# Performance work log

Hardware: AMD Instinct MI355X
Metric: run time of the kernel (lower is better)

The kernel has to match this reference:

```python
import jax, jax.numpy as jnp
import numpy as np

B, S, D, H = 2, 1024, 768, 12
HD = D // H          # head_dim = 64
DFF = 4 * D          # 3072
EPS = 1e-5


def _ln(x, g, b):
    m = x.mean(-1, keepdims=True)
    v = ((x - m) ** 2).mean(-1, keepdims=True)
    return (x - m) * jax.lax.rsqrt(v + EPS) * g + b


def setup_inputs() -> dict:
    key = jax.random.key(0)
    ks = jax.random.split(key, 8)
    w = lambda k, shape: jax.random.normal(k, shape, jnp.float32) * 0.02
    return {
        "inp": jax.random.normal(ks[0], (B, S, D), jnp.float32),
        "attention_mask": jnp.zeros((B, S), bool),  # True = masked out (filled with -inf)
        "rel_matrix": jax.random.randint(ks[1], (B, S, S), -1, 2, jnp.int32),  # values in {-1,0,1}
        "qkv_w": w(ks[2], (3 * D, D)),
        "rel_A": w(ks[3], (3, HD)),        # relative_position_emb_A.weight
        "o_w": w(ks[4], (D, D)),
        "w1": w(ks[5], (DFF, D)), "b1": jnp.zeros((DFF,), jnp.float32),
        "w2": w(ks[6], (D, DFF)), "b2": jnp.zeros((D,), jnp.float32),
        "ln1_g": jnp.ones((D,), jnp.float32), "ln1_b": jnp.zeros((D,), jnp.float32),
        "ln2_g": jnp.ones((D,), jnp.float32), "ln2_b": jnp.zeros((D,), jnp.float32),
    }


def reference(inp, attention_mask, rel_matrix, qkv_w, rel_A, o_w,
              w1, b1, w2, b2, ln1_g, ln1_b, ln2_g, ln2_b):
    x = _ln(inp, ln1_g, ln1_b)
    qkv = x @ qkv_w.T                                  # (B,S,3D)
    q, k, v = jnp.split(qkv, 3, axis=-1)
    heads = lambda t: t.reshape(B, S, H, HD).transpose(0, 2, 1, 3)  # (B,H,S,HD)
    q, k, v = heads(q), heads(k), heads(v)

    # q @ (k + rel_emb)^T without materializing k_aug:
    # q.k^T term plus per-(q,key) relative term gathered from q @ A^T.
    logits = jnp.einsum("bhqd,bhkd->bhqk", q, k)       # (B,H,S,S)
    r = jnp.einsum("bhqd,cd->bhqc", q, rel_A)          # (B,H,S,3)
    idx = (rel_matrix + 1).astype(jnp.int32)           # (B,S,S) in {0,1,2}
    rel = jnp.take_along_axis(r, jnp.broadcast_to(idx[:, None], (B, H, S, S)), axis=-1)
    logits = (logits + rel) / np.sqrt(HD).astype(np.float32)
    # masked_fill: -inf where mask is True
    logits = jnp.where(attention_mask[:, None, None, :], -jnp.inf, logits)

    attn = jax.nn.softmax(logits, axis=-1)
    out = jnp.einsum("bhqk,bhkd->bhqd", attn, v)
    out = out.transpose(0, 2, 1, 3).reshape(B, S, D)
    inp = inp + out @ o_w.T                            # residual (dropout=0)

    h = _ln(inp, ln2_g, ln2_b)
    mlp = jax.nn.relu(h @ w1.T + b1) @ w2.T + b2
    return inp + mlp
```

## Files before the change

kernel.cpp:

```cpp
#include <hip/hip_runtime.h>
#include <hip/hip_bf16.h>

#define BB 2
#define SS 1024
#define DD 768
#define HH 12
#define HD 64
#define DFF 3072
#define EPS 1e-5f
#define BS2 (BB * SS)
#define BSD ((size_t)BS2 * DD)

typedef unsigned short ushort_t;
typedef unsigned char uchar_t;
using short8 = __attribute__((ext_vector_type(8))) short;
using f32x4  = __attribute__((ext_vector_type(4))) float;

#define WAITCNT_LGKM0 0xC07F

__device__ __forceinline__ ushort_t f2bf_rne(float f) {
    union { float f; unsigned u; } x; x.f = f;
    unsigned r = x.u + 0x7fff + ((x.u >> 16) & 1);
    return (ushort_t)(r >> 16);
}
__device__ __forceinline__ float bf2f(short u) {
    union { unsigned i; float f; } x;
    x.i = ((unsigned)(ushort_t)u) << 16;
    return x.f;
}

#define CVT_N1 (3 * DD * DD / 4)
#define CVT_N2 (CVT_N1 + DD * DD / 4)
#define CVT_N3 (CVT_N2 + DFF * DD / 4)
#define CVT_NT (CVT_N3 + DD * DFF / 4)
#define PREP_CVT   (CVT_NT / 256)
#define PREP_CODES (BB * SS)
#define PREP_LN    BS2

__global__ __launch_bounds__(256) void prep_kernel(
    const float* __restrict__ qkv_w, const float* __restrict__ o_w,
    const float* __restrict__ w1, const float* __restrict__ w2,
    ushort_t* __restrict__ wdst,
    const int* __restrict__ rel, const uchar_t* __restrict__ mask,
    unsigned* __restrict__ codes,
    const float* __restrict__ x, const float* __restrict__ g,
    const float* __restrict__ b, ushort_t* __restrict__ y)
{
    const int bx = blockIdx.x;
    const int t  = threadIdx.x;
    if (bx < PREP_CVT) {
        int i = bx * 256 + t;
        const float* src; int off;
        if (i < CVT_N1)      { src = qkv_w; off = i; }
        else if (i < CVT_N2) { src = o_w;   off = i - CVT_N1; }
        else if (i < CVT_N3) { src = w1;    off = i - CVT_N2; }
        else                 { src = w2;    off = i - CVT_N3; }
        float4 v = ((const float4*)src)[off];
        ushort4 o;
        o.x = f2bf_rne(v.x); o.y = f2bf_rne(v.y);
        o.z = f2bf_rne(v.z); o.w = f2bf_rne(v.w);
        ((ushort4*)wdst)[i] = o;
        return;
    }
    if (bx < PREP_CVT + PREP_CODES) {
        int tid = (bx - PREP_CVT) * 256 + t;
        int l15 = tid & 15;
        int kt  = (tid >> 4) & 15;
        int q   = (tid >> 8) & (SS - 1);
        int bb  = tid >> 18;
        const int* rrow = rel + ((size_t)(bb * SS + q)) * SS + kt * 64 + l15;
        const uchar_t* mrow = mask + (size_t)bb * SS + kt * 64 + l15;
        unsigned o = 0;
#pragma unroll
        for (int nt = 0; nt < 4; ++nt) {
            unsigned c = mrow[nt * 16] ? 3u : (unsigned)(rrow[nt * 16] + 1);
            o |= c << (8 * nt);
        }
        codes[((size_t)(bb * SS + q) * 16 + kt) * 16 + l15] = o;
        return;
    }
    const int row = bx - PREP_CVT - PREP_CODES;
    const float* xr = x + (size_t)row * DD;
    float s = 0.f, ss = 0.f;
    for (int i = t; i < DD; i += 256) {
        float v = xr[i];
        s += v; ss += v * v;
    }
    for (int off = 32; off; off >>= 1) {
        s  += __shfl_down(s,  off);
        ss += __shfl_down(ss, off);
    }
    __shared__ float reds[4], redss[4], bc[2];
    if ((t & 63) == 0) { reds[t >> 6] = s; redss[t >> 6] = ss; }
    __syncthreads();
    if (t == 0) {
        float S1 = reds[0] + reds[1] + reds[2] + reds[3];
        float S2 = redss[0] + redss[1] + redss[2] + redss[3];
        float mean = S1 / DD;
        float var = S2 / DD - mean * mean;
        bc[0] = mean;
        bc[1] = rsqrtf(var + EPS);
    }
    __syncthreads();
    float mean = bc[0], inv = bc[1];
    ushort_t* yr = y + (size_t)row * DD;
    for (int i = t; i < DD; i += 256) {
        yr[i] = f2bf_rne((xr[i] - mean) * inv * g[i] + b[i]);
    }
}

__global__ __launch_bounds__(256) void merge2_ln_kernel(
    const ushort_t* __restrict__ part, const float* __restrict__ inp,
    const float* __restrict__ g, const float* __restrict__ b,
    float* __restrict__ resid, ushort_t* __restrict__ h_bf)
{
    const int row = blockIdx.x;
    const int t = threadIdx.x;
    float4 v = make_float4(0.f, 0.f, 0.f, 0.f);
    const size_t idx = (size_t)row * (DD / 4) + t;
    if (t < DD / 4) {
        v = ((const float4*)inp)[idx];
        ushort4 p0 = ((const ushort4*)part)[idx];
        ushort4 p1 = ((const ushort4*)(part + BSD))[idx];
        v.x += bf2f(p0.x) + bf2f(p1.x);
        v.y += bf2f(p0.y) + bf2f(p1.y);
        v.z += bf2f(p0.z) + bf2f(p1.z);
        v.w += bf2f(p0.w) + bf2f(p1.w);
        ((float4*)resid)[idx] = v;
    }
    float s  = v.x + v.y + v.z + v.w;
    float ss = v.x * v.x + v.y * v.y + v.z * v.z + v.w * v.w;
    for (int off = 32; off; off >>= 1) {
        s  += __shfl_down(s,  off);
        ss += __shfl_down(ss, off);
    }
    __shared__ float reds[4], redss[4], bc[2];
    if ((t & 63) == 0) { reds[t >> 6] = s; redss[t >> 6] = ss; }
    __syncthreads();
    if (t == 0) {
        float S1 = reds[0] + reds[1] + reds[2] + reds[3];
        float S2 = redss[0] + redss[1] + redss[2] + redss[3];
        float mean = S1 / DD;
        float var = S2 / DD - mean * mean;
        bc[0] = mean;
        bc[1] = rsqrtf(var + EPS);
    }
    __syncthreads();
    if (t < DD / 4) {
        const float mean = bc[0], inv = bc[1];
        float4 gv = ((const float4*)g)[t];
        float4 bv = ((const float4*)b)[t];
        ushort4 o;
        o.x = f2bf_rne((v.x - mean) * inv * gv.x + bv.x);
        o.y = f2bf_rne((v.y - mean) * inv * gv.y + bv.y);
        o.z = f2bf_rne((v.z - mean) * inv * gv.z + bv.z);
        o.w = f2bf_rne((v.w - mean) * inv * gv.w + bv.w);
        ((ushort4*)h_bf)[idx] = o;
    }
}

__global__ __launch_bounds__(256) void merge4_kernel(
    const ushort_t* __restrict__ part, const float* __restrict__ resid,
    const float* __restrict__ b2, float* __restrict__ outp, int n4)
{
    int i = blockIdx.x * 256 + threadIdx.x;
    if (i >= n4) return;
    float4 v = ((const float4*)resid)[i];
    int col4 = (i * 4) % DD;
    float4 bv = *(const float4*)(b2 + col4);
    v.x += bv.x; v.y += bv.y; v.z += bv.z; v.w += bv.w;
#pragma unroll
    for (int z = 0; z < 4; ++z) {
        ushort4 pz = ((const ushort4*)(part + (size_t)z * BSD))[i];
        v.x += bf2f(pz.x); v.y += bf2f(pz.y);
        v.z += bf2f(pz.z); v.w += bf2f(pz.w);
    }
    ((float4*)outp)[i] = v;
}

template <bool RELU, bool OUT_BF16, bool HAS_BIAS, bool PARTIAL>
__global__ __launch_bounds__(256) void gemm_tile(
    const ushort_t* __restrict__ A, const ushort_t* __restrict__ W,
    const float* __restrict__ bias, void* __restrict__ Cout,
    int M, int N, int K, int Ksplit)
{
    __shared__ __align__(16) ushort_t As[512 * 8];
    __shared__ __align__(16) ushort_t Bs[1024 * 8];

    const int t  = threadIdx.x;
    const int n0 = blockIdx.x * 128;
    const int m0 = blockIdx.y * 64;
    const int kb = blockIdx.z * Ksplit;
    const int w  = t >> 6;
    const int l  = t & 63;
    const int wm = (w & 1) * 32;
    const int wn = (w >> 1) * 64;
    const int l15  = l & 15;
    const int quad = l >> 4;

    const ushort_t* gA = A + (size_t)(m0 + (t & 63)) * K + kb + (t >> 6) * 8;
    const ushort_t* gB = W + (size_t)(n0 + (t & 127)) * K + kb + (t >> 7) * 8;

    short8 pa0 = *(const short8*)(gA);
    short8 pa1 = *(const short8*)(gA + 32);
    short8 pb0 = *(const short8*)(gB);
    short8 pb1 = *(const short8*)(gB + 16);
    short8 pb2 = *(const short8*)(gB + 32);
    short8 pb3 = *(const short8*)(gB + 48);

    f32x4 acc[2][4] = {};
    const int nIter = Ksplit >> 6;

    for (int it = 0; it < nIter; ++it) {
        __builtin_amdgcn_s_barrier();
        *(short8*)&As[(size_t)t * 8]           = pa0;
        *(short8*)&As[(size_t)(t + 256) * 8]   = pa1;
        *(short8*)&Bs[(size_t)t * 8]           = pb0;
        *(short8*)&Bs[(size_t)(t + 256) * 8]   = pb1;
        *(short8*)&Bs[(size_t)(t + 512) * 8]   = pb2;
        *(short8*)&Bs[(size_t)(t + 768) * 8]   = pb3;
        if (it + 1 < nIter) {
            const int k0 = (it + 1) << 6;
            pa0 = *(const short8*)(gA + k0);
            pa1 = *(const short8*)(gA + k0 + 32);
            pb0 = *(const short8*)(gB + k0);
            pb1 = *(const short8*)(gB + k0 + 16);
            pb2 = *(const short8*)(gB + k0 + 32);
            pb3 = *(const short8*)(gB + k0 + 48);
        }
        __builtin_amdgcn_s_waitcnt(WAITCNT_LGKM0);
        __builtin_amdgcn_s_barrier();

#pragma unroll
        for (int ks = 0; ks < 2; ++ks) {
            const ushort_t* aptr = &As[(size_t)((ks * 4 + quad) * 64 + wm + l15) * 8];
            const ushort_t* bptr = &Bs[(size_t)((ks * 4 + quad) * 128 + wn + l15) * 8];
            short8 af[2], bf[4];
#pragma unroll
            for (int i = 0; i < 2; ++i)
                af[i] = *(const short8*)(aptr + (size_t)i * 16 * 8);
#pragma unroll
            for (int j = 0; j < 4; ++j)
                bf[j] = *(const short8*)(bptr + (size_t)j * 16 * 8);
#pragma unroll
            for (int i = 0; i < 2; ++i)
#pragma unroll
                for (int j = 0; j < 4; ++j)
                    acc[i][j] = __builtin_amdgcn_mfma_f32_16x16x32_bf16(
                        af[i], bf[j], acc[i][j], 0, 0, 0);
        }
    }

    if (PARTIAL) {
        ushort_t* Cp = (ushort_t*)Cout + (size_t)blockIdx.z * ((size_t)M * N);
#pragma unroll
        for (int i = 0; i < 2; ++i) {
            const int row = m0 + wm + i * 16 + quad * 4;
#pragma unroll
            for (int j = 0; j < 4; ++j) {
                const int col = n0 + wn + j * 16 + l15;
#pragma unroll
                for (int r = 0; r < 4; ++r)
                    Cp[(size_t)(row + r) * N + col] = f2bf_rne(acc[i][j][r]);
            }
        }
    } else {
#pragma unroll
        for (int i = 0; i < 2; ++i) {
            const int row = m0 + wm + i * 16 + quad * 4;
#pragma unroll
            for (int j = 0; j < 4; ++j) {
                const int col = n0 + wn + j * 16 + l15;
                const float bv = HAS_BIAS ? bias[col] : 0.f;
#pragma unroll
                for (int r = 0; r < 4; ++r) {
                    float v = acc[i][j][r] + bv;
                    if (RELU) v = fmaxf(v, 0.f);
                    if (OUT_BF16)
                        ((ushort_t*)Cout)[(size_t)(row + r) * N + col] = f2bf_rne(v);
                    else
                        ((float*)Cout)[(size_t)(row + r) * N + col] = v;
                }
            }
        }
    }
}

__global__ __launch_bounds__(256) void attn_mfma_kernel(
    const ushort_t* __restrict__ qkv,
    const unsigned* __restrict__ codes,
    const float* __restrict__ rel_A,
    ushort_t* __restrict__ Opart,
    float* __restrict__ lpart)
{
    __shared__ __align__(16) ushort_t Ks[2][64 * 64];
    __shared__ __align__(16) unsigned Vt2[2][64 * 36];
    __shared__ __align__(16) ushort_t Ps[64 * 72];
    __shared__ __align__(16) float r3s[64][4];

    const int bx = blockIdx.x;
    const int ks = bx & 1;
    const int qt = (bx >> 1) & 15;
    const int h  = (bx >> 5) % HH;
    const int b  = bx / (32 * HH);
    const int q0 = qt * 64;
    const int t  = threadIdx.x;
    const int w  = t >> 6;
    const int l  = t & 63;
    const int l15  = l & 15;
    const int quad = l >> 4;

    const int sr  = t >> 3;
    const int scp = t & 7;
    const int vkp = t >> 3;
    const int vdg = t & 7;
    const int vkps = vkp ^ (vdg * 4);

    const size_t qrow = (size_t)(b * SS + q0 + w * 16 + l15) * (3 * DD) + h * HD;
    const short8 qf0 = *(const short8*)(qkv + qrow + quad * 8);
    const short8 qf1 = *(const short8*)(qkv + qrow + 32 + quad * 8);

    {
        float rv[3];
#pragma unroll
        for (int c = 0; c < 3; ++c) {
            const float* a = rel_A + c * HD + quad * 8;
            float acc = 0.f;
#pragma unroll
            for (int j = 0; j < 8; ++j) acc += bf2f(qf0[j]) * a[j];
#pragma unroll
            for (int j = 0; j < 8; ++j) acc += bf2f(qf1[j]) * a[32 + j];
            acc += __shfl_xor(acc, 16);
            acc += __shfl_xor(acc, 32);
            rv[c] = acc;
        }
        if (quad == 0) {
            float4 f4 = make_float4(rv[0], rv[1], rv[2], -2.4e31f);
            *(float4*)&r3s[w * 16 + l15][0] = f4;
        }
    }

    float l_run[4] = {0.f, 0.f, 0.f, 0.f};
    f32x4 oacc[4] = {};

    const int kt0 = ks * 8;
    short8 va, vb;
    {
        const int k0 = kt0 * 64;
        const int cl  = scp ^ (sr & 7);
        const ushort_t* g = qkv + (size_t)(b * SS + k0 + sr) * (3 * DD) + DD + h * HD + cl * 8;
        __builtin_amdgcn_global_load_lds(
            (const __attribute__((address_space(1))) unsigned*)g,
            (__attribute__((address_space(3))) unsigned*)(&Ks[0][0] + (size_t)t * 8), 16, 0, 0);
        const int r2  = sr + 32;
        const int cl2 = scp ^ (r2 & 7);
        const ushort_t* g2 = qkv + (size_t)(b * SS + k0 + r2) * (3 * DD) + DD + h * HD + cl2 * 8;
        __builtin_amdgcn_global_load_lds(
            (const __attribute__((address_space(1))) unsigned*)g2,
            (__attribute__((address_space(3))) unsigned*)(&Ks[0][0] + (size_t)(t + 256) * 8), 16, 0, 0);
        const ushort_t* gv = qkv + (size_t)(b * SS + k0 + 2 * vkp) * (3 * DD) + 2 * DD + h * HD + vdg * 8;
        va = *(const short8*)gv;
        vb = *(const short8*)(gv + 3 * DD);
#pragma unroll
        for (int i = 0; i < 8; ++i)
            Vt2[0][(size_t)(vdg * 8 + i) * 36 + vkps] =
                (unsigned)(ushort_t)va[i] | ((unsigned)(ushort_t)vb[i] << 16);
    }
    __syncthreads();
    float4 r3v[4];
#pragma unroll
    for (int reg = 0; reg < 4; ++reg)
        r3v[reg] = *(const float4*)&r3s[w * 16 + quad * 4 + reg][0];

    for (int i8 = 0; i8 < 8; ++i8) {
        const int kt  = kt0 + i8;
        const int cur = i8 & 1;
        const bool more = (i8 + 1 < 8);
        if (more) {
            const int k0 = (kt + 1) * 64;
            const int nb = cur ^ 1;
            const int cl  = scp ^ (sr & 7);
            const ushort_t* g = qkv + (size_t)(b * SS + k0 + sr) * (3 * DD) + DD + h * HD + cl * 8;
            __builtin_amdgcn_global_load_lds(
                (const __attribute__((address_space(1))) unsigned*)g,
                (__attribute__((address_space(3))) unsigned*)(&Ks[nb][0] + (size_t)t * 8), 16, 0, 0);
            const int r2  = sr + 32;
            const int cl2 = scp ^ (r2 & 7);
            const ushort_t* g2 = qkv + (size_t)(b * SS + k0 + r2) * (3 * DD) + DD + h * HD + cl2 * 8;
            __builtin_amdgcn_global_load_lds(
                (const __attribute__((address_space(1))) unsigned*)g2,
                (__attribute__((address_space(3))) unsigned*)(&Ks[nb][0] + (size_t)(t + 256) * 8), 16, 0, 0);
            const ushort_t* gv = qkv + (size_t)(b * SS + k0 + 2 * vkp) * (3 * DD) + 2 * DD + h * HD + vdg * 8;
            va = *(const short8*)gv;
            vb = *(const short8*)(gv + 3 * DD);
        }

        f32x4 sacc[4] = {};
#pragma unroll
        for (int kc = 0; kc < 2; ++kc) {
            const short8 qv = kc ? qf1 : qf0;
#pragma unroll
            for (int nt = 0; nt < 4; ++nt) {
                const int row = nt * 16 + l15;
                const int cp  = (kc * 4 + quad) ^ (row & 7);
                const short8 kf = *(const short8*)(&Ks[cur][0] + (size_t)row * 64 + cp * 8);
                sacc[nt] = __builtin_amdgcn_mfma_f32_16x16x32_bf16(qv, kf, sacc[nt], 0, 0, 0);
            }
        }

#pragma unroll
        for (int reg = 0; reg < 4; ++reg) {
            const int qloc = w * 16 + quad * 4 + reg;
            const unsigned cds = codes[((size_t)(b * SS + q0 + qloc) * 16 + kt) * 16 + l15];
            const float4 r4 = r3v[reg];
#pragma unroll
            for (int nt = 0; nt < 4; ++nt) {
                const unsigned c = (cds >> (8 * nt)) & 0xff;
                float rvv = (c == 0) ? r4.x : (c == 1) ? r4.y : (c == 2) ? r4.z : r4.w;
                const float p = __expf((sacc[nt][reg] + rvv) * 0.125f);
                l_run[reg] += p;
                Ps[(size_t)qloc * 72 + nt * 16 + l15] = f2bf_rne(p);
            }
        }

#pragma unroll
        for (int kc = 0; kc < 2; ++kc) {
            const short8 pf = *(const short8*)(Ps + (size_t)(w * 16 + l15) * 72 + kc * 32 + quad * 8);
#pragma unroll
            for (int dt = 0; dt < 4; ++dt) {
                const int d  = dt * 16 + l15;
                const int dg = d >> 3;
                const int kps0 = (kc * 16 + quad * 4) ^ ((dg & 7) * 4);
                const short8 vf = *(const short8*)((const ushort_t*)&Vt2[cur][(size_t)d * 36 + kps0]);
                oacc[dt] = __builtin_amdgcn_mfma_f32_16x16x32_bf16(pf, vf, oacc[dt], 0, 0, 0);
            }
        }

        if (more) {
            const int nb = cur ^ 1;
#pragma unroll
            for (int i = 0; i < 8; ++i)
                Vt2[nb][(size_t)(vdg * 8 + i) * 36 + vkps] =
                    (unsigned)(ushort_t)va[i] | ((unsigned)(ushort_t)vb[i] << 16);
            __syncthreads();
        }
    }

    ushort_t* Op = Opart + (size_t)ks * BSD;
    float* lp = lpart + (size_t)ks * BS2 * HH;
#pragma unroll
    for (int reg = 0; reg < 4; ++reg) {
        float ls = l_run[reg];
        ls += __shfl_xor(ls, 1);
        ls += __shfl_xor(ls, 2);
        ls += __shfl_xor(ls, 4);
        ls += __shfl_xor(ls, 8);
        const int orow = b * SS + q0 + w * 16 + quad * 4 + reg;
#pragma unroll
        for (int dt = 0; dt < 4; ++dt)
            Op[(size_t)orow * DD + h * HD + dt * 16 + l15] = f2bf_rne(oacc[dt][reg]);
        if (l15 == 0) lp[(size_t)orow * HH + h] = ls;
    }
}

__global__ __launch_bounds__(256) void attn_merge(
    const ushort_t* __restrict__ Opart, const float* __restrict__ lpart,
    ushort_t* __restrict__ att_bf)
{
    int i = blockIdx.x * 256 + threadIdx.x;
    int row = (i * 4) / DD;
    int h   = ((i * 4) % DD) >> 6;
    float l0 = lpart[(size_t)row * HH + h];
    float l1 = lpart[(size_t)BS2 * HH + (size_t)row * HH + h];
    float inv = 1.0f / (l0 + l1);
    ushort4 a = ((const ushort4*)Opart)[i];
    ushort4 b = ((const ushort4*)(Opart + BSD))[i];
    ushort4 o;
    o.x = f2bf_rne((bf2f(a.x) + bf2f(b.x)) * inv);
    o.y = f2bf_rne((bf2f(a.y) + bf2f(b.y)) * inv);
    o.z = f2bf_rne((bf2f(a.z) + bf2f(b.z)) * inv);
    o.w = f2bf_rne((bf2f(a.w) + bf2f(b.w)) * inv);
    ((ushort4*)att_bf)[i] = o;
}

extern "C" void kernel_launch(void* const* d_in, const int* in_sizes, int n_in,
                              void* d_out, int out_size, void* d_ws, size_t ws_size,
                              hipStream_t stream) {
    const float* inp   = (const float*)d_in[0];
    const uchar_t* amask = (const uchar_t*)d_in[1];
    const int*   relm  = (const int*)d_in[2];
    const float* qkv_w = (const float*)d_in[3];
    const float* rel_A = (const float*)d_in[4];
    const float* o_w   = (const float*)d_in[5];
    const float* w1    = (const float*)d_in[6];
    const float* b1    = (const float*)d_in[7];
    const float* w2    = (const float*)d_in[8];
    const float* b2    = (const float*)d_in[9];
    const float* ln1_g = (const float*)d_in[10];
    const float* ln1_b = (const float*)d_in[11];
    const float* ln2_g = (const float*)d_in[12];
    const float* ln2_b = (const float*)d_in[13];
    float* out = (float*)d_out;

    char* p = (char*)d_ws;
    ushort_t* x_bf   = (ushort_t*)p; p += BSD * 2;
    ushort_t* att_bf = (ushort_t*)p; p += BSD * 2;
    ushort_t* h_bf   = (ushort_t*)p; p += BSD * 2;
    ushort_t* ff_bf  = (ushort_t*)p; p += (size_t)BS2 * DFF * 2;
    ushort_t* qkvw_bf= (ushort_t*)p; p += (size_t)3 * DD * DD * 2;
    ushort_t* ow_bf  = (ushort_t*)p; p += (size_t)DD * DD * 2;
    ushort_t* w1_bf  = (ushort_t*)p; p += (size_t)DFF * DD * 2;
    ushort_t* w2_bf  = (ushort_t*)p; p += (size_t)DD * DFF * 2;
    ushort_t* qkv_bf = (ushort_t*)p; p += (size_t)BS2 * 3 * DD * 2;
    float*    resid  = (float*)p;    p += BSD * 4;
    ushort_t* pool   = (ushort_t*)p; p += 4 * BSD * 2;
    ushort_t* Opart  = (ushort_t*)p; p += 2 * BSD * 2;
    float*    lpart  = (float*)p;    p += (size_t)2 * BS2 * HH * 4;
    unsigned* codes  = (unsigned*)p; p += (size_t)BB * SS * SS;

    prep_kernel<<<PREP_CVT + PREP_CODES + PREP_LN, 256, 0, stream>>>(
        qkv_w, o_w, w1, w2, qkvw_bf, relm, amask, codes,
        inp, ln1_g, ln1_b, x_bf);

    gemm_tile<false, true, false, false>
        <<<dim3(3 * DD / 128, BS2 / 64, 1), 256, 0, stream>>>(
        x_bf, qkvw_bf, nullptr, qkv_bf, BS2, 3 * DD, DD, DD);

    attn_mfma_kernel<<<BB * HH * 16 * 2, 256, 0, stream>>>(
        qkv_bf, codes, rel_A, Opart, lpart);
    attn_merge<<<(int)(BSD / 4 / 256), 256, 0, stream>>>(Opart, lpart, att_bf);

    gemm_tile<false, false, false, true>
        <<<dim3(DD / 128, BS2 / 64, 2), 256, 0, stream>>>(
        att_bf, ow_bf, nullptr, pool, BS2, DD, DD, DD / 2);

    merge2_ln_kernel<<<BS2, 256, 0, stream>>>(
        pool, inp, ln2_g, ln2_b, resid, h_bf);

    gemm_tile<true, true, true, false>
        <<<dim3(DFF / 128, BS2 / 64, 1), 256, 0, stream>>>(
        h_bf, w1_bf, b1, ff_bf, BS2, DFF, DD, DD);

    gemm_tile<false, false, false, true>
        <<<dim3(DD / 128, BS2 / 64, 4), 256, 0, stream>>>(
        ff_bf, w2_bf, nullptr, pool, BS2, DD, DFF, DFF / 4);

    merge4_kernel<<<(int)(BSD / 4 / 256), 256, 0, stream>>>(
        pool, resid, b2, out, (int)(BSD / 4));
}
```

Baseline: 255.7 us.

## Use direct global-to-LDS loads and enlarge GEMM tile to 128x128

The GEMM kernel swaps its register-prefetch double buffering for global_load_lds direct-to-LDS transfers and doubles the M tile from 64 to 128, so each wave computes a 64x64 sub-tile with twice as many MFMAs per LDS load. This aims to cut register staging and raise data reuse per K step. In exchange, loads are no longer overlapped with compute (a single buffer with barriers), and the grid halves, leaving fewer blocks to fill the CUs, notably for the split-K O-projection and W2 GEMMs.

```diff
diff --git a/kernel.cpp b/kernel.cpp
--- a/kernel.cpp
+++ b/kernel.cpp
@@ -184,77 +184,68 @@
     const float* __restrict__ bias, void* __restrict__ Cout,
     int M, int N, int K, int Ksplit)
 {
-    __shared__ __align__(16) ushort_t As[512 * 8];
+    __shared__ __align__(16) ushort_t As[1024 * 8];
     __shared__ __align__(16) ushort_t Bs[1024 * 8];
 
     const int t  = threadIdx.x;
     const int n0 = blockIdx.x * 128;
-    const int m0 = blockIdx.y * 64;
+    const int m0 = blockIdx.y * 128;
     const int kb = blockIdx.z * Ksplit;
     const int w  = t >> 6;
     const int l  = t & 63;
-    const int wm = (w & 1) * 32;
+    const int wm = (w & 1) * 64;
     const int wn = (w >> 1) * 64;
     const int l15  = l & 15;
     const int quad = l >> 4;
 
-    const ushort_t* gA = A + (size_t)(m0 + (t & 63)) * K + kb + (t >> 6) * 8;
-    const ushort_t* gB = W + (size_t)(n0 + (t & 127)) * K + kb + (t >> 7) * 8;
-
-    short8 pa0 = *(const short8*)(gA);
-    short8 pa1 = *(const short8*)(gA + 32);
-    short8 pb0 = *(const short8*)(gB);
-    short8 pb1 = *(const short8*)(gB + 16);
-    short8 pb2 = *(const short8*)(gB + 32);
-    short8 pb3 = *(const short8*)(gB + 48);
-
-    f32x4 acc[2][4] = {};
+    const int rowT = t & 127;
+    const int kq0  = t >> 7;
+    const ushort_t* gA = A + (size_t)(m0 + rowT) * K + kb + kq0 * 8;
+    const ushort_t* gB = W + (size_t)(n0 + rowT) * K + kb + kq0 * 8;
+
+    f32x4 acc[4][4] = {};
     const int nIter = Ksplit >> 6;
 
     for (int it = 0; it < nIter; ++it) {
-        __builtin_amdgcn_s_barrier();
-        *(short8*)&As[(size_t)t * 8]           = pa0;
-        *(short8*)&As[(size_t)(t + 256) * 8]   = pa1;
-        *(short8*)&Bs[(size_t)t * 8]           = pb0;
-        *(short8*)&Bs[(size_t)(t + 256) * 8]   = pb1;
-        *(short8*)&Bs[(size_t)(t + 512) * 8]   = pb2;
-        *(short8*)&Bs[(size_t)(t + 768) * 8]   = pb3;
-        if (it + 1 < nIter) {
-            const int k0 = (it + 1) << 6;
-            pa0 = *(const short8*)(gA + k0);
-            pa1 = *(const short8*)(gA + k0 + 32);
-            pb0 = *(const short8*)(gB + k0);
-            pb1 = *(const short8*)(gB + k0 + 16);
-            pb2 = *(const short8*)(gB + k0 + 32);
-            pb3 = *(const short8*)(gB + k0 + 48);
-        }
-        __builtin_amdgcn_s_waitcnt(WAITCNT_LGKM0);
-        __builtin_amdgcn_s_barrier();
+        const int k0 = it << 6;
+#pragma unroll
+        for (int j = 0; j < 4; ++j) {
+            __builtin_amdgcn_global_load_lds(
+                (const __attribute__((address_space(1))) unsigned*)(gA + k0 + j * 16),
+                (__attribute__((address_space(3))) unsigned*)(&As[(size_t)(j * 256 + t) * 8]),
+                16, 0, 0);
+            __builtin_amdgcn_global_load_lds(
+                (const __attribute__((address_space(1))) unsigned*)(gB + k0 + j * 16),
+                (__attribute__((address_space(3))) unsigned*)(&Bs[(size_t)(j * 256 + t) * 8]),
+                16, 0, 0);
+        }
+        __syncthreads();
 
 #pragma unroll
         for (int ks = 0; ks < 2; ++ks) {
-            const ushort_t* aptr = &As[(size_t)((ks * 4 + quad) * 64 + wm + l15) * 8];
+            const ushort_t* aptr = &As[(size_t)((ks * 4 + quad) * 128 + wm + l15) * 8];
             const ushort_t* bptr = &Bs[(size_t)((ks * 4 + quad) * 128 + wn + l15) * 8];
-            short8 af[2], bf[4];
-#pragma unroll
-            for (int i = 0; i < 2; ++i)
+            short8 af[4], bf[4];
+#pragma unroll
+            for (int i = 0; i < 4; ++i)
                 af[i] = *(const short8*)(aptr + (size_t)i * 16 * 8);
 #pragma unroll
             for (int j = 0; j < 4; ++j)
                 bf[j] = *(const short8*)(bptr + (size_t)j * 16 * 8);
 #pragma unroll
-            for (int i = 0; i < 2; ++i)
+            for (int i = 0; i < 4; ++i)
 #pragma unroll
                 for (int j = 0; j < 4; ++j)
                     acc[i][j] = __builtin_amdgcn_mfma_f32_16x16x32_bf16(
                         af[i], bf[j], acc[i][j], 0, 0, 0);
         }
+        if (it + 1 < nIter) __syncthreads();
     }
 
     if (PARTIAL) {
         ushort_t* Cp = (ushort_t*)Cout + (size_t)blockIdx.z * ((size_t)M * N);
 #pragma unroll
-        for (int i = 0; i < 2; ++i) {
+        for (int i = 0; i < 4; ++i) {
             const int row = m0 + wm + i * 16 + quad * 4;
 #pragma unroll
             for (int j = 0; j < 4; ++j) {
@@ -266,7 +257,7 @@
         }
     } else {
 #pragma unroll
-        for (int i = 0; i < 2; ++i) {
+        for (int i = 0; i < 4; ++i) {
             const int row = m0 + wm + i * 16 + quad * 4;
 #pragma unroll
             for (int j = 0; j < 4; ++j) {
@@ -523,7 +514,7 @@
         inp, ln1_g, ln1_b, x_bf);
 
     gemm_tile<false, true, false, false>
-        <<<dim3(3 * DD / 128, BS2 / 64, 1), 256, 0, stream>>>(
+        <<<dim3(3 * DD / 128, BS2 / 128, 1), 256, 0, stream>>>(
         x_bf, qkvw_bf, nullptr, qkv_bf, BS2, 3 * DD, DD, DD);
 
     attn_mfma_kernel<<<BB * HH * 16 * 2, 256, 0, stream>>>(
@@ -531,18 +522,18 @@
     attn_merge<<<(int)(BSD / 4 / 256), 256, 0, stream>>>(Opart, lpart, att_bf);
 
     gemm_tile<false, false, false, true>
-        <<<dim3(DD / 128, BS2 / 64, 2), 256, 0, stream>>>(
+        <<<dim3(DD / 128, BS2 / 128, 2), 256, 0, stream>>>(
         att_bf, ow_bf, nullptr, pool, BS2, DD, DD, DD / 2);
 
     merge2_ln_kernel<<<BS2, 256, 0, stream>>>(
         pool, inp, ln2_g, ln2_b, resid, h_bf);
 
     gemm_tile<true, true, true, false>
-        <<<dim3(DFF / 128, BS2 / 64, 1), 256, 0, stream>>>(
+        <<<dim3(DFF / 128, BS2 / 128, 1), 256, 0, stream>>>(
         h_bf, w1_bf, b1, ff_bf, BS2, DFF, DD, DD);
 
     gemm_tile<false, false, false, true>
-        <<<dim3(DD / 128, BS2 / 64, 4), 256, 0, stream>>>(
+        <<<dim3(DD / 128, BS2 / 128, 4), 256, 0, stream>>>(
         ff_bf, w2_bf, nullptr, pool, BS2, DD, DFF, DFF / 4);
 
     merge4_kernel<<<(int)(BSD / 4 / 256), 256, 0, stream>>>(
```

After: 268.3 us. +4.9%, slower.
